# Optimization experiments

Hardware: AMD Instinct MI355X
Metric: run time of the kernel (lower is better)

Reference implementation:

```python
import jax, jax.numpy as jnp
import numpy as np

DIM = 768
NUM_HEADS = 12
HEAD_DIM = DIM // NUM_HEADS
SCALE = HEAD_DIM ** -0.5
NEG = -9e15


def setup_inputs() -> dict:
    key = jax.random.key(0)
    ks = jax.random.split(key, 8)
    B, N, M, C = 4, 1024, 2048, DIM
    q = jax.random.normal(ks[0], (B, N, C), dtype=jnp.float32)
    kv = jax.random.normal(ks[1], (B, M, C), dtype=jnp.float32)
    mask = jax.random.randint(ks[2], (B, 1, N, M), 0, 2, dtype=jnp.int32)
    s = 1.0 / np.sqrt(C)
    Wq = jax.random.normal(ks[3], (C, C), dtype=jnp.float32) * s      # nn.Linear(dim, dim), no bias
    Wkv = jax.random.normal(ks[4], (2 * C, C), dtype=jnp.float32) * s  # nn.Linear(dim, 2*dim), no bias
    Wproj = jax.random.normal(ks[5], (C, C), dtype=jnp.float32) * s
    bproj = jax.random.normal(ks[6], (C,), dtype=jnp.float32) * s
    return {"q": q, "kv": kv, "Wq": Wq, "Wkv": Wkv, "Wproj": Wproj, "bproj": bproj, "mask": mask}


def reference(q, kv, Wq, Wkv, Wproj, bproj, mask):
    B, M, C = kv.shape
    _, N, _ = q.shape
    H, d = NUM_HEADS, HEAD_DIM
    # kv projection -> [B, M, 2, H, d] -> k, v: [B, H, M, d]
    kvp = (kv @ Wkv.T).reshape(B, M, 2, H, d)
    k = kvp[:, :, 0].transpose(0, 2, 1, 3)
    v = kvp[:, :, 1].transpose(0, 2, 1, 3)
    # q projection -> [B, H, N, d], pre-scaled
    qp = (q @ Wq.T).reshape(B, N, H, d).transpose(0, 2, 1, 3) * SCALE
    attn = jnp.einsum('bhnd,bhmd->bhnm', qp, k)  # [B, H, N, M]
    attn = jnp.where(mask == 0, NEG, attn)
    attn = jax.nn.softmax(attn, axis=-1)
    # attn_drop / proj_drop have rate 0.0 (eval): identity
    x = jnp.einsum('bhnm,bhmd->bhnd', attn, v)
    x = x.transpose(0, 2, 1, 3).reshape(B, N, C)
    x = x @ Wproj.T + bproj
    return x
```

## Files before the change

kernel.cpp:

```cpp
#include <hip/hip_runtime.h>
#include <hip/hip_bf16.h>


typedef short    s16x8  __attribute__((ext_vector_type(8)));
typedef short    s16x4  __attribute__((ext_vector_type(4)));
typedef float    f32x4  __attribute__((ext_vector_type(4)));
typedef _Float16 f16x8  __attribute__((ext_vector_type(8)));
typedef _Float16 f16x4  __attribute__((ext_vector_type(4)));
typedef _Float16 f16x2  __attribute__((ext_vector_type(2)));

#define NUM_H 12
#define DIM   768
#define NQ    1024
#define MK    2048
#define QK_SCALE_LOG2E 0.18033688f

__device__ __forceinline__ short f2h(float v) {
    _Float16 h = (_Float16)v;
    return __builtin_bit_cast(short, h);
}
__device__ __forceinline__ f32x4 mfma16x32(f16x8 a, f16x8 b, f32x4 c) {
    return __builtin_amdgcn_mfma_f32_16x16x32_f16(a, b, c, 0, 0, 0);
}
__device__ __forceinline__ f16x2 pk2h(float a, float b) {
    return __builtin_bit_cast(f16x2, __builtin_amdgcn_cvt_pkrtz(a, b));
}

__global__ __launch_bounds__(256) void prep_kernel(
    const float* __restrict__ q, const float* __restrict__ kv,
    const float* __restrict__ Wq, const float* __restrict__ Wkv,
    const float* __restrict__ Wp, const int* __restrict__ mask,
    short* __restrict__ q_h, short* __restrict__ kv_h,
    short* __restrict__ Wq_h, short* __restrict__ Wkv_h,
    short* __restrict__ Wp_h, unsigned char* __restrict__ mbytes)
{
    int bid = blockIdx.x;
    if (bid < 5760) {
        const float* s; short* d; long base;
        if (bid < 1536)      { s = q;   d = q_h;   base = (long)bid * 2048; }
        else if (bid < 4608) { s = kv;  d = kv_h;  base = (long)(bid - 1536) * 2048; }
        else if (bid < 4896) { s = Wq;  d = Wq_h;  base = (long)(bid - 4608) * 2048; }
        else if (bid < 5472) { s = Wkv; d = Wkv_h; base = (long)(bid - 4896) * 2048; }
        else                 { s = Wp;  d = Wp_h;  base = (long)(bid - 5472) * 2048; }
        long i = base + threadIdx.x * 8;
        float4 a = *(const float4*)(s + i);
        float4 b = *(const float4*)(s + i + 4);
        s16x8 r;
        r[0] = f2h(a.x); r[1] = f2h(a.y); r[2] = f2h(a.z); r[3] = f2h(a.w);
        r[4] = f2h(b.x); r[5] = f2h(b.y); r[6] = f2h(b.z); r[7] = f2h(b.w);
        *(s16x8*)(d + i) = r;
    } else {
        long base = (long)(bid - 5760) * 2048 + threadIdx.x * 8;
        int4 m0 = *(const int4*)(mask + base);
        int4 m1 = *(const int4*)(mask + base + 4);
        unsigned v = (unsigned)(m0.x != 0)        | ((unsigned)(m0.y != 0) << 1)
                   | ((unsigned)(m0.z != 0) << 2) | ((unsigned)(m0.w != 0) << 3)
                   | ((unsigned)(m1.x != 0) << 4) | ((unsigned)(m1.y != 0) << 5)
                   | ((unsigned)(m1.z != 0) << 6) | ((unsigned)(m1.w != 0) << 7);
        mbytes[base >> 3] = (unsigned char)v;
    }
}

__device__ __forceinline__ void gemm_core(
    short* smem,
    const short* __restrict__ A, const short* __restrict__ Bt,
    int Ncols, int mode, const float* __restrict__ bias,
    short* __restrict__ outb, short* __restrict__ outb2,
    float* __restrict__ outf, int bid)
{
    short (*As)[72] = (short(*)[72])smem;
    short (*Bs)[72] = (short(*)[72])(smem + 9216);

    int ntiles = Ncols >> 7;
    int m0 = (bid / ntiles) << 7;
    int n0 = (bid % ntiles) << 7;
    int t = threadIdx.x;
    int w = t >> 6, lane = t & 63, quad = lane >> 4, l16 = lane & 15;
    int wm = (w & 1) << 6, wn = (w >> 1) << 6;

    f32x4 zero4 = {0.f, 0.f, 0.f, 0.f};
    f32x4 acc[4][4];
    for (int i = 0; i < 4; i++)
        for (int j = 0; j < 4; j++) acc[i][j] = zero4;

    int lr = t >> 1;
    int lc = (t & 1) << 5;
    const short* Ap = A + (long)(m0 + lr) * DIM + lc;
    const short* Bp = Bt + (long)(n0 + lr) * DIM + lc;

    s16x8 a8[4], b8[4];
    #pragma unroll
    for (int c = 0; c < 4; c++) {
        a8[c] = *(const s16x8*)(Ap + c * 8);
        b8[c] = *(const s16x8*)(Bp + c * 8);
    }

    for (int kt = 0; kt < DIM; kt += 64) {
        __syncthreads();
        #pragma unroll
        for (int c = 0; c < 4; c++) {
            *(s16x8*)&As[lr][lc + c * 8] = a8[c];
            *(s16x8*)&Bs[lr][lc + c * 8] = b8[c];
        }
        __syncthreads();
        if (kt + 64 < DIM) {
            #pragma unroll
            for (int c = 0; c < 4; c++) {
                a8[c] = *(const s16x8*)(Ap + kt + 64 + c * 8);
                b8[c] = *(const s16x8*)(Bp + kt + 64 + c * 8);
            }
        }
        #pragma unroll
        for (int kh = 0; kh < 2; kh++) {
            f16x8 af[4], bfr[4];
            #pragma unroll
            for (int i = 0; i < 4; i++) {
                s16x8 tmp = *(const s16x8*)&As[wm + i * 16 + l16][kh * 32 + quad * 8];
                af[i] = __builtin_bit_cast(f16x8, tmp);
            }
            #pragma unroll
            for (int j = 0; j < 4; j++) {
                s16x8 tmp = *(const s16x8*)&Bs[wn + j * 16 + l16][kh * 32 + quad * 8];
                bfr[j] = __builtin_bit_cast(f16x8, tmp);
            }
            #pragma unroll
            for (int i = 0; i < 4; i++)
                #pragma unroll
                for (int j = 0; j < 4; j++)
                    acc[i][j] = mfma16x32(af[i], bfr[j], acc[i][j]);
        }
    }

    __syncthreads();

    if (mode == 2) {
        #pragma unroll
        for (int i = 0; i < 4; i++)
            #pragma unroll
            for (int j = 0; j < 4; j++)
                #pragma unroll
                for (int r = 0; r < 4; r++) {
                    int row = m0 + wm + i * 16 + quad * 4 + r;
                    int col = n0 + wn + j * 16 + l16;
                    outf[(long)row * DIM + col] = acc[i][j][r] + bias[col];
                }
        return;
    }

    short (*Cs)[136] = (short(*)[136])smem;
    bool vreg = (mode == 1) && (n0 >= DIM);

    if (!vreg) {
        float sc = (mode == 0) ? QK_SCALE_LOG2E : 1.0f;
        #pragma unroll
        for (int i = 0; i < 4; i++)
            #pragma unroll
            for (int j = 0; j < 4; j++)
                #pragma unroll
                for (int r = 0; r < 4; r++)
                    Cs[wm + i * 16 + quad * 4 + r][wn + j * 16 + l16] =
                        f2h(acc[i][j][r] * sc);
    } else {
        #pragma unroll
        for (int i = 0; i < 4; i++)
            #pragma unroll
            for (int j = 0; j < 4; j++) {
                int c = wn + j * 16 + l16;
                int r0 = wm + i * 16 + quad * 4;
                s16x4 pk;
                pk[0] = f2h(acc[i][j][0]); pk[1] = f2h(acc[i][j][1]);
                pk[2] = f2h(acc[i][j][2]); pk[3] = f2h(acc[i][j][3]);
                *(s16x4*)&Cs[c][r0] = pk;
            }
    }
    __syncthreads();

    if (!vreg) {
        int hb2 = n0 >> 6;
        long rowsN = (mode == 0) ? NQ : MK;
        int b = (int)(m0 / rowsN);
        int rb = (int)(m0 % rowsN);
        short* ob0 = outb + ((long)(b * NUM_H + hb2) * rowsN + rb) * 64;
        short* ob1 = outb + ((long)(b * NUM_H + hb2 + 1) * rowsN + rb) * 64;
        #pragma unroll
        for (int k2 = 0; k2 < 8; k2++) {
            int ch = k2 * 256 + t;
            int half = ch >> 10, off = ch & 1023;
            s16x8 vd = *(const s16x8*)&Cs[off >> 3][(half << 6) + ((off & 7) << 3)];
            *(s16x8*)((half ? ob1 : ob0) + off * 8) = vd;
        }
    } else {
        int hb2 = (n0 - DIM) >> 6;
        int b = m0 >> 11, rb = m0 & 2047;
        #pragma unroll
        for (int k2 = 0; k2 < 8; k2++) {
            int ch = k2 * 256 + t;
            int c = ch >> 4, woff = (ch & 15) << 3;
            s16x8 vd = *(const s16x8*)&Cs[c][woff];
            int half = c >> 6, dd = c & 63;
            *(s16x8*)(outb2 + (((long)(b * NUM_H + hb2 + half) * 64 + dd) * MK + rb) + woff) = vd;
        }
    }
}

__global__ __launch_bounds__(256) void gemm12_kernel(
    const short* __restrict__ qh, const short* __restrict__ Wqh,
    const short* __restrict__ kvh, const short* __restrict__ Wkvh,
    short* __restrict__ qp, short* __restrict__ kk, short* __restrict__ vt)
{
    __shared__ short smem[18432];
    if (blockIdx.x < 192)
        gemm_core(smem, qh, Wqh, 768, 0, nullptr, qp, nullptr, nullptr, blockIdx.x);
    else
        gemm_core(smem, kvh, Wkvh, 1536, 1, nullptr, kk, vt, nullptr, blockIdx.x - 192);
}

__global__ __launch_bounds__(256) void gemm3_kernel(
    const short* __restrict__ xb, const short* __restrict__ Wph,
    const float* __restrict__ bias, float* __restrict__ out)
{
    __shared__ short smem[18432];
    gemm_core(smem, xb, Wph, 768, 2, bias, nullptr, nullptr, out, blockIdx.x);
}

__global__ __launch_bounds__(256) void attn_kernel(
    const short* __restrict__ qp, const short* __restrict__ kk,
    const short* __restrict__ vt, const unsigned* __restrict__ mb,
    short* __restrict__ xb)
{
    __shared__ short qs[64][72];
    __shared__ short ks[64][72];
    __shared__ short vs[64][72];

    int bid = blockIdx.x;
    int bh = bid % 48;
    int nt = bid / 48;
    int h = bh % NUM_H, b = bh / NUM_H;
    int n0 = nt << 6;
    int t = threadIdx.x, w = t >> 6, lane = t & 63, quad = lane >> 4, l16 = lane & 15;

    const short* qbase = qp + ((long)bh * NQ + n0) * 64;
    const short* kbase = kk + (long)bh * MK * 64;
    const short* vbase = vt + (long)bh * 64 * MK;
    const unsigned* mrow = mb + ((long)b * NQ + n0 + (w << 4) + l16) * 64;

    {
        int qr = t >> 2, c0 = (t & 3) << 4;
        *(s16x8*)&qs[qr][c0]     = *(const s16x8*)(qbase + qr * 64 + c0);
        *(s16x8*)&qs[qr][c0 + 8] = *(const s16x8*)(qbase + qr * 64 + c0 + 8);
    }
    __syncthreads();
    f16x8 bq[2];
    #pragma unroll
    for (int kh = 0; kh < 2; kh++)
        bq[kh] = __builtin_bit_cast(f16x8,
            *(const s16x8*)&qs[(w << 4) + l16][kh * 32 + quad * 8]);

    int sr = t >> 2, c0 = (t & 3) << 4;
    int pr = (sr & 32) + ((sr & 4) << 2) + ((sr & 24) >> 1) + (sr & 3);
    const short* kp = kbase + (long)sr * 64 + c0;
    const short* vp = vbase + (long)sr * MK + c0;

    s16x8 k0 = *(const s16x8*)(kp);
    s16x8 k1 = *(const s16x8*)(kp + 8);
    s16x8 v0 = *(const s16x8*)(vp);
    s16x8 v1 = *(const s16x8*)(vp + 8);
    uint2 mwv = *(const uint2*)(mrow);

    f32x4 zero4 = {0.f, 0.f, 0.f, 0.f};
    f32x4 o[4], ol = zero4;
    for (int j = 0; j < 4; j++) o[j] = zero4;
    const f16x8 ones = {(_Float16)1.f, (_Float16)1.f, (_Float16)1.f, (_Float16)1.f,
                        (_Float16)1.f, (_Float16)1.f, (_Float16)1.f, (_Float16)1.f};

    for (int mt = 0; mt < MK; mt += 64) {
        __syncthreads();
        *(s16x8*)&ks[pr][c0]     = k0;
        *(s16x8*)&ks[pr][c0 + 8] = k1;
        *(s16x8*)&vs[sr][c0]     = v0;
        *(s16x8*)&vs[sr][c0 + 8] = v1;
        unsigned cm0 = mwv.x, cm1 = mwv.y;
        __syncthreads();
        if (mt + 64 < MK) {
            k0 = *(const s16x8*)(kp + (long)(mt + 64) * 64);
            k1 = *(const s16x8*)(kp + (long)(mt + 64) * 64 + 8);
            v0 = *(const s16x8*)(vp + mt + 64);
            v1 = *(const s16x8*)(vp + mt + 64 + 8);
            mwv = *(const uint2*)(mrow + ((mt + 64) >> 5));
        }

        f32x4 s[4];
        #pragma unroll
        for (int jj = 0; jj < 4; jj++) s[jj] = zero4;
        #pragma unroll
        for (int kh = 0; kh < 2; kh++)
            #pragma unroll
            for (int jj = 0; jj < 4; jj++) {
                f16x8 ak = __builtin_bit_cast(f16x8,
                    *(const s16x8*)&ks[jj * 16 + l16][kh * 32 + quad * 8]);
                s[jj] = mfma16x32(ak, bq[kh], s[jj]);
            }

        f16x8 pa[2];
        #pragma unroll
        for (int j2 = 0; j2 < 2; j2++) {
            unsigned wsel = j2 ? cm1 : cm0;
            f16x2 pk[4];
            #pragma unroll
            for (int sub = 0; sub < 2; sub++) {
                unsigned bits = wsel >> ((quad << 3) + (sub << 2));
                const f32x4& sv = s[j2 * 2 + sub];
                float p0 = (bits & 1u)        ? __builtin_amdgcn_exp2f(sv[0]) : 0.f;
                float p1 = ((bits >> 1) & 1u) ? __builtin_amdgcn_exp2f(sv[1]) : 0.f;
                float p2 = ((bits >> 2) & 1u) ? __builtin_amdgcn_exp2f(sv[2]) : 0.f;
                float p3 = ((bits >> 3) & 1u) ? __builtin_amdgcn_exp2f(sv[3]) : 0.f;
                pk[sub * 2]     = pk2h(p0, p1);
                pk[sub * 2 + 1] = pk2h(p2, p3);
            }
            f16x4 lo = __builtin_shufflevector(pk[0], pk[1], 0, 1, 2, 3);
            f16x4 hi = __builtin_shufflevector(pk[2], pk[3], 0, 1, 2, 3);
            pa[j2] = __builtin_shufflevector(lo, hi, 0, 1, 2, 3, 4, 5, 6, 7);
        }

        #pragma unroll
        for (int j2 = 0; j2 < 2; j2++) {
            ol = mfma16x32(pa[j2], ones, ol);
            #pragma unroll
            for (int jd = 0; jd < 4; jd++) {
                f16x8 bv = __builtin_bit_cast(f16x8,
                    *(const s16x8*)&vs[jd * 16 + l16][j2 * 32 + quad * 8]);
                o[jd] = mfma16x32(pa[j2], bv, o[jd]);
            }
        }
    }

    float linv[4];
    #pragma unroll
    for (int rr = 0; rr < 4; rr++) linv[rr] = 1.0f / ol[rr];
    short (*ps)[72] = (short(*)[72])&qs[w << 4];
    #pragma unroll
    for (int jd = 0; jd < 4; jd++)
        #pragma unroll
        for (int rr = 0; rr < 4; rr++)
            ps[quad * 4 + rr][jd * 16 + l16] = f2h(o[jd][rr] * linv[rr]);

    #pragma unroll
    for (int k2 = 0; k2 < 2; k2++) {
        int row = (lane >> 3) + k2 * 8;
        int cc = (lane & 7) << 3;
        s16x8 vd = *(const s16x8*)&ps[row][cc];
        *(s16x8*)(xb + ((long)b * NQ + n0 + (w << 4) + row) * DIM + h * 64 + cc) = vd;
    }
}

extern "C" void kernel_launch(void* const* d_in, const int* in_sizes, int n_in,
                              void* d_out, int out_size, void* d_ws, size_t ws_size,
                              hipStream_t stream)
{
    const float* q     = (const float*)d_in[0];
    const float* kv    = (const float*)d_in[1];
    const float* Wq    = (const float*)d_in[2];
    const float* Wkv   = (const float*)d_in[3];
    const float* Wproj = (const float*)d_in[4];
    const float* bproj = (const float*)d_in[5];
    const int*   mask  = (const int*)d_in[6];
    float* out = (float*)d_out;

    char* ws = (char*)d_ws;
    short* q_h   = (short*)ws; ws += (size_t)4096 * 768 * 2;
    short* kv_h  = (short*)ws; ws += (size_t)8192 * 768 * 2;
    short* Wq_h  = (short*)ws; ws += (size_t)768 * 768 * 2;
    short* Wkv_h = (short*)ws; ws += (size_t)1536 * 768 * 2;
    short* Wp_h  = (short*)ws; ws += (size_t)768 * 768 * 2;
    short* qp    = (short*)ws; ws += (size_t)4096 * 768 * 2;
    short* kk    = (short*)ws; ws += (size_t)8192 * 768 * 2;
    short* vt    = (short*)ws; ws += (size_t)8192 * 768 * 2;
    short* xb    = (short*)ws; ws += (size_t)4096 * 768 * 2;
    unsigned char* mbytes = (unsigned char*)ws;

    prep_kernel<<<9856, 256, 0, stream>>>(q, kv, Wq, Wkv, Wproj, mask,
                                          q_h, kv_h, Wq_h, Wkv_h, Wp_h, mbytes);
    gemm12_kernel<<<960, 256, 0, stream>>>(q_h, Wq_h, kv_h, Wkv_h, qp, kk, vt);
    attn_kernel<<<768, 256, 0, stream>>>(qp, kk, vt, (const unsigned*)mbytes, xb);
    gemm3_kernel<<<192, 256, 0, stream>>>(xb, Wp_h, bproj, out);
}
```

Baseline: 216.4 us.

## Split attention key range across 8 waves with LDS atomic reduction

The attention kernel now launches 512 threads per block and splits each 64-key tile among 4 waves along the key axis, with 2 query-row groups. Each wave loads its K fragment straight into registers instead of staging it through shared memory, and V is double-buffered in LDS with one barrier per tile. Partial outputs and row sums are reduced across waves with shared-memory float atomics at the end, and the row sums are kept in scalar accumulators rather than computed by an MFMA against ones. The aim is more waves in flight and less LDS traffic per tile, at the cost of a final atomic reduction and a larger block.

```diff
diff --git a/kernel.cpp b/kernel.cpp
--- a/kernel.cpp
+++ b/kernel.cpp
@@ -21,6 +21,9 @@
 }
 __device__ __forceinline__ f32x4 mfma16x32(f16x8 a, f16x8 b, f32x4 c) {
     return __builtin_amdgcn_mfma_f32_16x16x32_f16(a, b, c, 0, 0, 0);
+}
+__device__ __forceinline__ f32x4 mfma16x16(f16x4 a, f16x4 b, f32x4 c) {
+    return __builtin_amdgcn_mfma_f32_16x16x16f16(a, b, c, 0, 0, 0);
 }
 __device__ __forceinline__ f16x2 pk2h(float a, float b) {
     return __builtin_bit_cast(f16x2, __builtin_amdgcn_cvt_pkrtz(a, b));
@@ -223,133 +226,143 @@
     gemm_core(smem, xb, Wph, 768, 2, bias, nullptr, nullptr, out, blockIdx.x);
 }
 
-__global__ __launch_bounds__(256) void attn_kernel(
+__global__ __launch_bounds__(512, 4) void attn_kernel(
     const short* __restrict__ qp, const short* __restrict__ kk,
-    const short* __restrict__ vt, const unsigned* __restrict__ mb,
+    const short* __restrict__ vt, const unsigned char* __restrict__ mb,
     short* __restrict__ xb)
 {
-    __shared__ short qs[64][72];
-    __shared__ short ks[64][72];
-    __shared__ short vs[64][72];
+    __shared__ char smem[27648];
+    short (*qs)[72]  = (short(*)[72])smem;
+    short (*vb0)[72] = (short(*)[72])(smem + 9216);
+    short (*vb1)[72] = (short(*)[72])(smem + 18432);
+    float* Racc = (float*)smem;
+    float* lacc = (float*)(smem + 17408);
 
     int bid = blockIdx.x;
-    int bh = bid % 48;
-    int nt = bid / 48;
+    int bh = bid % 48, nt = bid / 48;
     int h = bh % NUM_H, b = bh / NUM_H;
     int n0 = nt << 6;
-    int t = threadIdx.x, w = t >> 6, lane = t & 63, quad = lane >> 4, l16 = lane & 15;
+    int t = threadIdx.x;
+    int w = t >> 6, lane = t & 63, quad = lane >> 4, l16 = lane & 15;
+    int wm = w & 3, wq = w >> 2;
 
     const short* qbase = qp + ((long)bh * NQ + n0) * 64;
     const short* kbase = kk + (long)bh * MK * 64;
     const short* vbase = vt + (long)bh * 64 * MK;
-    const unsigned* mrow = mb + ((long)b * NQ + n0 + (w << 4) + l16) * 64;
+
+    int gr = t >> 3, gc = (t & 7) << 3;
+
+    *(s16x8*)&qs[gr][gc] = *(const s16x8*)(qbase + gr * 64 + gc);
+    const short* vptr = vbase + (long)gr * MK + gc;
+    *(s16x8*)&vb0[gr][gc] = *(const s16x8*)(vptr);
+    s16x8 vnext = *(const s16x8*)(vptr + 64);
+    const short* kptr = kbase + (long)(wm * 16 + l16) * 64 + quad * 8;
+    s16x8 kreg0 = *(const s16x8*)(kptr);
+    s16x8 kreg1 = *(const s16x8*)(kptr + 32);
+    const unsigned char* mrow0 =
+        mb + ((long)(b * NQ + n0 + wq * 32 + l16) << 8) + (wm << 1);
+    const unsigned char* mrow1 = mrow0 + (16 << 8);
+    unsigned cmk0 = *(const unsigned short*)(mrow0);
+    unsigned cmk1 = *(const unsigned short*)(mrow1);
+    __syncthreads();
+
+    f16x8 bq[2][2];
+    #pragma unroll
+    for (int q2 = 0; q2 < 2; q2++)
+        #pragma unroll
+        for (int kh = 0; kh < 2; kh++)
+            bq[q2][kh] = __builtin_bit_cast(f16x8,
+                *(const s16x8*)&qs[wq * 32 + q2 * 16 + l16][kh * 32 + quad * 8]);
+
+    f32x4 zero4 = {0.f, 0.f, 0.f, 0.f};
+    f32x4 o[2][4];
+    float lsum0 = 0.f, lsum1 = 0.f;
+    #pragma unroll
+    for (int q2 = 0; q2 < 2; q2++)
+        for (int jd = 0; jd < 4; jd++) o[q2][jd] = zero4;
+
+    for (int tt = 0; tt < 32; tt++) {
+        int mt = tt << 6;
+        short (*cur)[72] = (tt & 1) ? vb1 : vb0;
+        short (*nxt)[72] = (tt & 1) ? vb0 : vb1;
+
+        f16x8 ak0 = __builtin_bit_cast(f16x8, kreg0);
+        f16x8 ak1 = __builtin_bit_cast(f16x8, kreg1);
+        f32x4 s0 = zero4, s1 = zero4;
+        s0 = mfma16x32(ak0, bq[0][0], s0);
+        s0 = mfma16x32(ak1, bq[0][1], s0);
+        s1 = mfma16x32(ak0, bq[1][0], s1);
+        s1 = mfma16x32(ak1, bq[1][1], s1);
+
+        unsigned bits0 = cmk0 >> (quad << 2);
+        unsigned bits1 = cmk1 >> (quad << 2);
+
+        if (tt < 31) {
+            kreg0 = *(const s16x8*)(kptr + (long)(mt + 64) * 64);
+            kreg1 = *(const s16x8*)(kptr + (long)(mt + 64) * 64 + 32);
+            cmk0 = *(const unsigned short*)(mrow0 + ((mt + 64) >> 3));
+            cmk1 = *(const unsigned short*)(mrow1 + ((mt + 64) >> 3));
+            *(s16x8*)&nxt[gr][gc] = vnext;
+            if (tt < 30) vnext = *(const s16x8*)(vptr + mt + 128);
+        }
+
+        float e0 = (bits0 & 1u)        ? __builtin_amdgcn_exp2f(s0[0]) : 0.f;
+        float e1 = ((bits0 >> 1) & 1u) ? __builtin_amdgcn_exp2f(s0[1]) : 0.f;
+        float e2 = ((bits0 >> 2) & 1u) ? __builtin_amdgcn_exp2f(s0[2]) : 0.f;
+        float e3 = ((bits0 >> 3) & 1u) ? __builtin_amdgcn_exp2f(s0[3]) : 0.f;
+        lsum0 += (e0 + e1) + (e2 + e3);
+        f16x2 lo0 = pk2h(e0, e1), hi0 = pk2h(e2, e3);
+        f16x4 pa0 = __builtin_shufflevector(lo0, hi0, 0, 1, 2, 3);
+        float f0 = (bits1 & 1u)        ? __builtin_amdgcn_exp2f(s1[0]) : 0.f;
+        float f1 = ((bits1 >> 1) & 1u) ? __builtin_amdgcn_exp2f(s1[1]) : 0.f;
+        float f2 = ((bits1 >> 2) & 1u) ? __builtin_amdgcn_exp2f(s1[2]) : 0.f;
+        float f3 = ((bits1 >> 3) & 1u) ? __builtin_amdgcn_exp2f(s1[3]) : 0.f;
+        lsum1 += (f0 + f1) + (f2 + f3);
+        f16x2 lo1 = pk2h(f0, f1), hi1 = pk2h(f2, f3);
+        f16x4 pa1 = __builtin_shufflevector(lo1, hi1, 0, 1, 2, 3);
+
+        #pragma unroll
+        for (int jd = 0; jd < 4; jd++) {
+            f16x4 bv = *(const f16x4*)&cur[jd * 16 + l16][(wm << 4) + (quad << 2)];
+            o[0][jd] = mfma16x16(pa0, bv, o[0][jd]);
+            o[1][jd] = mfma16x16(pa1, bv, o[1][jd]);
+        }
+        __syncthreads();
+    }
+
+    lsum0 += __shfl_xor(lsum0, 16); lsum0 += __shfl_xor(lsum0, 32);
+    lsum1 += __shfl_xor(lsum1, 16); lsum1 += __shfl_xor(lsum1, 32);
+
+    for (int i = t; i < 1104; i += 512)
+        *(f32x4*)(Racc + i * 4) = zero4;
+    __syncthreads();
+
+    #pragma unroll
+    for (int q2 = 0; q2 < 2; q2++)
+        #pragma unroll
+        for (int jd = 0; jd < 4; jd++)
+            #pragma unroll
+            for (int rr = 0; rr < 4; rr++) {
+                int qrow = wq * 32 + q2 * 16 + quad * 4 + rr;
+                atomicAdd(&Racc[qrow * 68 + jd * 16 + l16], o[q2][jd][rr]);
+            }
+    if (quad == 0) {
+        atomicAdd(&lacc[wq * 32 + l16], lsum0);
+        atomicAdd(&lacc[wq * 32 + 16 + l16], lsum1);
+    }
+    __syncthreads();
 
     {
-        int qr = t >> 2, c0 = (t & 3) << 4;
-        *(s16x8*)&qs[qr][c0]     = *(const s16x8*)(qbase + qr * 64 + c0);
-        *(s16x8*)&qs[qr][c0 + 8] = *(const s16x8*)(qbase + qr * 64 + c0 + 8);
-    }
-    __syncthreads();
-    f16x8 bq[2];
-    #pragma unroll
-    for (int kh = 0; kh < 2; kh++)
-        bq[kh] = __builtin_bit_cast(f16x8,
-            *(const s16x8*)&qs[(w << 4) + l16][kh * 32 + quad * 8]);
-
-    int sr = t >> 2, c0 = (t & 3) << 4;
-    int pr = (sr & 32) + ((sr & 4) << 2) + ((sr & 24) >> 1) + (sr & 3);
-    const short* kp = kbase + (long)sr * 64 + c0;
-    const short* vp = vbase + (long)sr * MK + c0;
-
-    s16x8 k0 = *(const s16x8*)(kp);
-    s16x8 k1 = *(const s16x8*)(kp + 8);
-    s16x8 v0 = *(const s16x8*)(vp);
-    s16x8 v1 = *(const s16x8*)(vp + 8);
-    uint2 mwv = *(const uint2*)(mrow);
-
-    f32x4 zero4 = {0.f, 0.f, 0.f, 0.f};
-    f32x4 o[4], ol = zero4;
-    for (int j = 0; j < 4; j++) o[j] = zero4;
-    const f16x8 ones = {(_Float16)1.f, (_Float16)1.f, (_Float16)1.f, (_Float16)1.f,
-                        (_Float16)1.f, (_Float16)1.f, (_Float16)1.f, (_Float16)1.f};
-
-    for (int mt = 0; mt < MK; mt += 64) {
-        __syncthreads();
-        *(s16x8*)&ks[pr][c0]     = k0;
-        *(s16x8*)&ks[pr][c0 + 8] = k1;
-        *(s16x8*)&vs[sr][c0]     = v0;
-        *(s16x8*)&vs[sr][c0 + 8] = v1;
-        unsigned cm0 = mwv.x, cm1 = mwv.y;
-        __syncthreads();
-        if (mt + 64 < MK) {
-            k0 = *(const s16x8*)(kp + (long)(mt + 64) * 64);
-            k1 = *(const s16x8*)(kp + (long)(mt + 64) * 64 + 8);
-            v0 = *(const s16x8*)(vp + mt + 64);
-            v1 = *(const s16x8*)(vp + mt + 64 + 8);
-            mwv = *(const uint2*)(mrow + ((mt + 64) >> 5));
-        }
-
-        f32x4 s[4];
-        #pragma unroll
-        for (int jj = 0; jj < 4; jj++) s[jj] = zero4;
-        #pragma unroll
-        for (int kh = 0; kh < 2; kh++)
-            #pragma unroll
-            for (int jj = 0; jj < 4; jj++) {
-                f16x8 ak = __builtin_bit_cast(f16x8,
-                    *(const s16x8*)&ks[jj * 16 + l16][kh * 32 + quad * 8]);
-                s[jj] = mfma16x32(ak, bq[kh], s[jj]);
-            }
-
-        f16x8 pa[2];
-        #pragma unroll
-        for (int j2 = 0; j2 < 2; j2++) {
-            unsigned wsel = j2 ? cm1 : cm0;
-            f16x2 pk[4];
-            #pragma unroll
-            for (int sub = 0; sub < 2; sub++) {
-                unsigned bits = wsel >> ((quad << 3) + (sub << 2));
-                const f32x4& sv = s[j2 * 2 + sub];
-                float p0 = (bits & 1u)        ? __builtin_amdgcn_exp2f(sv[0]) : 0.f;
-                float p1 = ((bits >> 1) & 1u) ? __builtin_amdgcn_exp2f(sv[1]) : 0.f;
-                float p2 = ((bits >> 2) & 1u) ? __builtin_amdgcn_exp2f(sv[2]) : 0.f;
-                float p3 = ((bits >> 3) & 1u) ? __builtin_amdgcn_exp2f(sv[3]) : 0.f;
-                pk[sub * 2]     = pk2h(p0, p1);
-                pk[sub * 2 + 1] = pk2h(p2, p3);
-            }
-            f16x4 lo = __builtin_shufflevector(pk[0], pk[1], 0, 1, 2, 3);
-            f16x4 hi = __builtin_shufflevector(pk[2], pk[3], 0, 1, 2, 3);
-            pa[j2] = __builtin_shufflevector(lo, hi, 0, 1, 2, 3, 4, 5, 6, 7);
-        }
-
-        #pragma unroll
-        for (int j2 = 0; j2 < 2; j2++) {
-            ol = mfma16x32(pa[j2], ones, ol);
-            #pragma unroll
-            for (int jd = 0; jd < 4; jd++) {
-                f16x8 bv = __builtin_bit_cast(f16x8,
-                    *(const s16x8*)&vs[jd * 16 + l16][j2 * 32 + quad * 8]);
-                o[jd] = mfma16x32(pa[j2], bv, o[jd]);
-            }
-        }
-    }
-
-    float linv[4];
-    #pragma unroll
-    for (int rr = 0; rr < 4; rr++) linv[rr] = 1.0f / ol[rr];
-    short (*ps)[72] = (short(*)[72])&qs[w << 4];
-    #pragma unroll
-    for (int jd = 0; jd < 4; jd++)
-        #pragma unroll
-        for (int rr = 0; rr < 4; rr++)
-            ps[quad * 4 + rr][jd * 16 + l16] = f2h(o[jd][rr] * linv[rr]);
-
-    #pragma unroll
-    for (int k2 = 0; k2 < 2; k2++) {
-        int row = (lane >> 3) + k2 * 8;
-        int cc = (lane & 7) << 3;
-        s16x8 vd = *(const s16x8*)&ps[row][cc];
-        *(s16x8*)(xb + ((long)b * NQ + n0 + (w << 4) + row) * DIM + h * 64 + cc) = vd;
+        int row = t >> 3, c8 = (t & 7) << 3;
+        f32x4 va = *(const f32x4*)&Racc[row * 68 + c8];
+        f32x4 vb = *(const f32x4*)&Racc[row * 68 + c8 + 4];
+        float linv = 1.0f / lacc[row];
+        s16x8 outv;
+        outv[0] = f2h(va[0] * linv); outv[1] = f2h(va[1] * linv);
+        outv[2] = f2h(va[2] * linv); outv[3] = f2h(va[3] * linv);
+        outv[4] = f2h(vb[0] * linv); outv[5] = f2h(vb[1] * linv);
+        outv[6] = f2h(vb[2] * linv); outv[7] = f2h(vb[3] * linv);
+        *(s16x8*)(xb + ((long)b * NQ + n0 + row) * DIM + h * 64 + c8) = outv;
     }
 }
 
@@ -381,6 +394,6 @@
     prep_kernel<<<9856, 256, 0, stream>>>(q, kv, Wq, Wkv, Wproj, mask,
                                           q_h, kv_h, Wq_h, Wkv_h, Wp_h, mbytes);
     gemm12_kernel<<<960, 256, 0, stream>>>(q_h, Wq_h, kv_h, Wkv_h, qp, kk, vt);
-    attn_kernel<<<768, 256, 0, stream>>>(qp, kk, vt, (const unsigned*)mbytes, xb);
+    attn_kernel<<<768, 512, 0, stream>>>(qp, kk, vt, mbytes, xb);
     gemm3_kernel<<<192, 256, 0, stream>>>(xb, Wp_h, bproj, out);
 }
```

New measurement: 318.4 us. 47.2% more time.
